# Kernel optimization log

Measured on AMD Instinct MI355X. Metric: run time of the kernel, lower is better.

## Reference

```python
import jax, jax.numpy as jnp
import numpy as np

KSIZE = 3; STRIDE = 1; RATE = 2; FUSE_K = 3; SCALE = 10.0; EPS = 1e-4
B, C, RH, RW = 2, 128, 80, 80  # raw (full-res) feature shape


def setup_inputs() -> dict:
    key = jax.random.key(0)
    ks = jax.random.split(key, 5)
    shp = (B, C, RH, RW)
    names = ["left", "right", "mid", "raw_left", "raw_right"]
    return {n: jax.random.normal(k, shp, dtype=jnp.float32) for n, k in zip(names, ks)}


def _same_pads(H, W, k, s):
    oh, ow = -(-H // s), -(-W // s)
    ph = max(0, (oh - 1) * s + k - H)
    pw = max(0, (ow - 1) * s + k - W)
    return ((ph // 2, ph - ph // 2), (pw // 2, pw - pw // 2))


def extract_patches(x, k, s):
    # torch extract_image_patches with 'same' padding -> (b, L, c, k, k)
    b, c, H, W = x.shape
    pads = _same_pads(H, W, k, s)
    p = jax.lax.conv_general_dilated_patches(x, (k, k), (s, s), pads)  # (b, c*k*k, oh, ow)
    oh, ow = p.shape[2], p.shape[3]
    p = p.reshape(b, c, k, k, oh * ow)  # feature dim is channel-major (c, k, k), like torch unfold
    return p.transpose(0, 4, 1, 2, 3)


def _fuse(s, Hl, Wl, Hm, Wm):
    # diagonal fuse-conv: conv of (b,1,L,P) score image with eye(k), twice with transposes
    b = s.shape[0]
    k = FUSE_K
    eye = jnp.eye(k, dtype=s.dtype).reshape(1, 1, k, k)
    pad = ((k // 2, k // 2), (k // 2, k // 2))
    conv = lambda x: jax.lax.conv_general_dilated(x, eye, (1, 1), pad)
    x = conv(s.reshape(b, 1, Hl * Wl, Hm * Wm))
    x = x.reshape(b, Hl, Wl, Hm, Wm).transpose(0, 2, 1, 4, 3).reshape(b, 1, Wl * Hl, Wm * Hm)
    x = conv(x)
    x = x.reshape(b, Wl, Hl, Wm, Hm).transpose(0, 2, 1, 4, 3)  # (b, Hl, Wl, Hm, Wm)
    return x.reshape(b, Hl * Wl, Hm, Wm)


def _deconv_one(attn, patches):
    # torch conv_transpose2d(attn, patches, stride=RATE, padding=1):
    # conv with lhs dilation RATE, spatially-flipped kernel, padding k-1-1
    kk = patches.shape[-1]
    rhs = jnp.flip(patches, (-2, -1)).transpose(1, 0, 2, 3)  # (C, L, kk, kk)
    p = kk - 1 - 1
    out = jax.lax.conv_general_dilated(attn[None], rhs, (1, 1), ((p, p), (p, p)),
                                       lhs_dilation=(RATE, RATE),
                                       dimension_numbers=('NCHW', 'OIHW', 'NCHW'))
    return out[0]


def _forward(left, right, mid, raw_left, raw_right):
    kernel = 2 * RATE
    rawp_l = extract_patches(raw_left, kernel, RATE * STRIDE)   # (B, L, C, 4, 4)
    rawp_r = extract_patches(raw_right, kernel, RATE * STRIDE)
    # nearest downsample by rate
    l = left[:, :, ::RATE, ::RATE]
    r = right[:, :, ::RATE, ::RATE]
    m = mid[:, :, ::RATE, ::RATE]
    Hl, Wl = l.shape[2], l.shape[3]
    Hm, Wm = m.shape[2], m.shape[3]
    lp = extract_patches(l, KSIZE, STRIDE)   # (B, L, C, 3, 3)
    rp = extract_patches(r, KSIZE, STRIDE)
    mp = extract_patches(m, KSIZE, STRIDE)   # (B, P, C, 3, 3); conv2d(same-padded xi, w) == patch dot

    def norm(p):
        # torch: sqrt(reduce_sum(p^2 + eps)) -- eps added elementwise before the sum
        return p / jnp.sqrt(jnp.sum(p * p + EPS, axis=(2, 3, 4), keepdims=True))

    sl = jnp.einsum('bqcij,bpcij->bqp', norm(lp), mp).reshape(-1, Hl * Wl, Hm, Wm)
    sr = jnp.einsum('bqcij,bpcij->bqp', norm(rp), mp).reshape(-1, Hl * Wl, Hm, Wm)
    sl = _fuse(sl, Hl, Wl, Hm, Wm)
    sr = _fuse(sr, Hl, Wl, Hm, Wm)
    al = jax.nn.softmax(sl * SCALE, axis=1)
    ar = jax.nn.softmax(sr * SCALE, axis=1)
    y_l = jax.vmap(_deconv_one)(al, rawp_l) / 4.0   # (B, C, RH, RW)
    y_r = jax.vmap(_deconv_one)(ar, rawp_r) / 4.0
    # cos_function_weight: cosine blending ramp along width (1 at left edge -> 0 at right edge)
    w = 0.5 * (1.0 + jnp.cos(jnp.pi * jnp.arange(RW, dtype=y_l.dtype) / (RW - 1)))
    w = w.reshape(1, 1, 1, RW)
    return w * y_l + jnp.flip(w, 3) * y_r


def reference(left, right, mid, raw_left, raw_right):
    return _forward(left, right, mid, raw_left, raw_right)
```

## Files before the change

kernel.cpp:

```cpp
#include <hip/hip_runtime.h>
#include <hip/hip_bf16.h>

typedef __hip_bfloat16 bf16;
typedef __attribute__((ext_vector_type(8))) short short8;
typedef __attribute__((ext_vector_type(4))) float f32x4;
typedef float f32x4u __attribute__((ext_vector_type(4), aligned(4)));
typedef unsigned short ushort_t;

#define PI_F 3.14159265358979323846f
#define GPAD_Z 3111696L

#define GLOAD_LDS16(gp, lp)                                                    \
  __builtin_amdgcn_global_load_lds(                                            \
      (const __attribute__((address_space(1))) unsigned int*)(gp),             \
      (__attribute__((address_space(3))) unsigned int*)(lp), 16, 0, 0)

__global__ __launch_bounds__(128) void prep_pt(const float* __restrict__ left,
                                               const float* __restrict__ right,
                                               const float* __restrict__ mid,
                                               bf16* __restrict__ PTe,
                                               bf16* __restrict__ MTe,
                                               float* __restrict__ SQ) {
  int q = blockIdx.x;
  int y = blockIdx.y;
  int c = threadIdx.x;
  int qi = q / 40, qj = q - qi * 40;
  const float* src;
  bf16* dst;
  int b;
  bool aside = (y < 4);
  if (aside) {
    b = y & 1;
    src = (y < 2) ? left : right;
    dst = PTe + (long)y * 1664 * 384;
  } else {
    b = y - 4;
    src = mid;
    dst = MTe + (long)(y - 4) * 1664 * 384;
  }
  float v = src[(((long)b * 128 + c) * 80 + 2 * qi) * 80 + 2 * qj];
  bf16 hi = __float2bfloat16(v);
  bf16 lo = __float2bfloat16(v - __bfloat162float(hi));
  if (aside) {
    dst[(long)q * 384 + c] = hi;
    dst[(long)q * 384 + 128 + c] = lo;
    dst[(long)q * 384 + 256 + c] = hi;
  } else {
    dst[(long)q * 384 + c] = hi;
    dst[(long)q * 384 + 128 + c] = hi;
    dst[(long)q * 384 + 256 + c] = lo;
  }
  if (aside) {
    __shared__ float red[128];
    red[c] = v * v;
    __syncthreads();
    for (int s = 64; s > 0; s >>= 1) {
      if (c < s) red[c] += red[c + s];
      __syncthreads();
    }
    if (c == 0) SQ[y * 1600 + q] = red[0];
  }
}

__global__ __launch_bounds__(256) void pad_invn_kernel(float* __restrict__ Gp,
                                                       const float* __restrict__ SQ,
                                                       float* __restrict__ INV) {
  int z = blockIdx.y;
  int bx = blockIdx.x;
  if (bx < 1764) {
    float* R = Gp + (long)z * GPAD_Z + (long)bx * 1764;
    int r42 = bx % 42;
    if (r42 == 0 || r42 == 41) {
      for (int c = threadIdx.x; c < 1764; c += 256) R[c] = 0.f;
    } else {
      for (int i = threadIdx.x; i < 84; i += 256) {
        int c = (i >> 1) * 42 + ((i & 1) ? 41 : 0);
        R[c] = 0.f;
      }
    }
  } else {
    int q = (bx - 1764) * 256 + threadIdx.x;
    if (q < 1600) {
      int qi = q / 40, qj = q - qi * 40;
      float s = 0.1152f;
      #pragma unroll
      for (int di = -1; di <= 1; ++di)
        #pragma unroll
        for (int dj = -1; dj <= 1; ++dj) {
          int a = qi + di, b2 = qj + dj;
          if (a >= 0 && a < 40 && b2 >= 0 && b2 < 40) s += SQ[z * 1600 + a * 40 + b2];
        }
      INV[z * 1600 + q] = rsqrtf(s);
    }
  }
}

__global__ __launch_bounds__(256) void gemm_nt(const bf16* __restrict__ A,
                                               const bf16* __restrict__ B,
                                               float* __restrict__ C,
                                               int M, int N, int K,
                                               long Az, long Bz, long Cz,
                                               int bmod, int cpad) {
  int z = blockIdx.z;
  A += (long)z * Az;
  B += (long)(bmod ? (z & 1) : z) * Bz;
  C += (long)z * Cz;
  __shared__ bf16 As[128 * 32];
  __shared__ bf16 Bs[128 * 32];
  int lane = threadIdx.x & 63;
  int w = threadIdx.x >> 6;
  int mb = blockIdx.x * 128;
  int nb = blockIdx.y * 128;
  int lr = lane >> 2;
  int gb = (lane & 3) ^ ((lane >> 3) & 3);
  int lm = lane & 15;
  int swz = (lm >> 1) & 3;
  int kb = lane >> 4;
  int pos = (kb ^ swz) * 8;
  int warow = (w >> 1) * 64;
  int wbrow = (w & 1) * 64;
  f32x4 acc[4][4];
  #pragma unroll
  for (int i = 0; i < 4; ++i)
    #pragma unroll
    for (int j = 0; j < 4; ++j) {
      f32x4 zv = {0.f, 0.f, 0.f, 0.f};
      acc[i][j] = zv;
    }
  for (int k0 = 0; k0 < K; k0 += 32) {
    __syncthreads();
    #pragma unroll
    for (int t = 0; t < 2; ++t) {
      int r = (w * 2 + t) * 16 + lr;
      GLOAD_LDS16(A + (long)(mb + r) * K + k0 + gb * 8, As + (w * 2 + t) * 512);
      GLOAD_LDS16(B + (long)(nb + r) * K + k0 + gb * 8, Bs + (w * 2 + t) * 512);
    }
    __syncthreads();
    short8 af[4], bfr[4];
    #pragma unroll
    for (int i = 0; i < 4; ++i) {
      af[i]  = *reinterpret_cast<const short8*>(As + (warow + i * 16 + lm) * 32 + pos);
      bfr[i] = *reinterpret_cast<const short8*>(Bs + (wbrow + i * 16 + lm) * 32 + pos);
    }
    #pragma unroll
    for (int i = 0; i < 4; ++i)
      #pragma unroll
      for (int j = 0; j < 4; ++j)
        acc[i][j] = __builtin_amdgcn_mfma_f32_16x16x32_bf16(af[i], bfr[j], acc[i][j], 0, 0, 0);
  }
  int m0 = mb + warow;
  int n0 = nb + wbrow;
  int col = lane & 15;
  int r0 = (lane >> 4) * 4;
  #pragma unroll
  for (int i = 0; i < 4; ++i)
    #pragma unroll
    for (int j = 0; j < 4; ++j) {
      int n = n0 + j * 16 + col;
      if (n < N) {
        int nc = cpad ? ((n / 40) * 42 + (n - (n / 40) * 40) + 43) : n;
        #pragma unroll
        for (int r = 0; r < 4; ++r) {
          int m = m0 + i * 16 + r0 + r;
          if (m < M) {
            long mr = cpad ? ((long)((m / 40) * 42 + (m - (m / 40) * 40) + 43) * 1764)
                           : ((long)m * N);
            C[mr + nc] = acc[i][j][r];
          }
        }
      }
    }
}

#define BAR() __builtin_amdgcn_s_barrier()
#define LGKM0() asm volatile("s_waitcnt lgkmcnt(0)" ::: "memory")
#define STAGE_A(tt, h)                                                         \
  { long _k = (long)(tt) * 64;                                                 \
    char* _d = lds + (((tt) & 1) << 16) + (((h) * 8 + w) << 11);               \
    GLOAD_LDS16(a_row[h] + _k, _d);                                            \
    GLOAD_LDS16(a_row[h] + _k + 32, _d + 1024); }
#define STAGE_B(tt, h)                                                         \
  { long _k = (long)(tt) * 64;                                                 \
    char* _d = lds + (((tt) & 1) << 16) + 32768 + (((h) * 8 + w) << 11);       \
    GLOAD_LDS16(b_row[h] + _k, _d);                                            \
    GLOAD_LDS16(b_row[h] + _k + 32, _d + 1024); }
#define LD8(off) (*reinterpret_cast<const short8*>(lds + (off)))
#define LOAD_A(dst, bufo, mh)                                                  \
  { _Pragma("unroll") for (int i = 0; i < 4; ++i)                              \
      { _Pragma("unroll") for (int kc = 0; kc < 2; ++kc)                       \
          dst[i][kc] = LD8((bufo) + (((wm * 8 + (mh) * 4 + i) * 2 + kc) << 10) + rd_off); } }
#define LOAD_B(dst, bufo, nh)                                                  \
  { _Pragma("unroll") for (int j = 0; j < 2; ++j)                              \
      { _Pragma("unroll") for (int kc = 0; kc < 2; ++kc)                       \
          dst[j][kc] = LD8((bufo) + 32768 + (((wn * 4 + (nh) * 2 + j) * 2 + kc) << 10) + rd_off); } }
#define MFMA16(arr, mh, nh, bset)                                              \
  { _Pragma("unroll") for (int kc = 0; kc < 2; ++kc)                           \
      { _Pragma("unroll") for (int i = 0; i < 4; ++i)                          \
          { _Pragma("unroll") for (int j = 0; j < 2; ++j)                      \
              acc[(mh) * 4 + i][(nh) * 2 + j] = __builtin_amdgcn_mfma_f32_16x16x32_bf16( \
                  arr[i][kc], bset[j][kc], acc[(mh) * 4 + i][(nh) * 2 + j], 0, 0, 0); } } }

__global__ __launch_bounds__(512, 2) void gemm256_nt(const bf16* __restrict__ A,
                                                     const bf16* __restrict__ B,
                                                     float* __restrict__ C,
                                                     int M, int N, int K,
                                                     long Az, long Bz, long Cz,
                                                     int nballoc) {
  __shared__ __align__(16) char lds[131072];
  int l = blockIdx.x + (blockIdx.y << 3) + blockIdx.z * 56;
  int x = l & 7;
  int j7 = l >> 3;
  int z = x >> 1;
  int mb = (((x & 1) << 2) + (j7 & 3)) * 256;
  int nb = (j7 >> 2) * 256;
  A += (long)z * Az;
  B += (long)z * Bz;
  C += (long)z * Cz;
  int tid = threadIdx.x;
  int lane = tid & 63;
  int w = tid >> 6;
  int wm = w >> 2;
  int wn = w & 3;
  int NT = K >> 6;

  int srcb = (lane << 4) ^ (lane & 32);
  int r_src = srcb >> 6;
  int c_src = (srcb & 63) >> 1;
  const bf16* a_row[2];
  const bf16* b_row[2];
  #pragma unroll
  for (int h = 0; h < 2; ++h) {
    a_row[h] = A + (long)(mb + (h * 8 + w) * 16 + r_src) * K + c_src;
    int br = nb + (h * 8 + w) * 16 + r_src;
    if (br > nballoc - 1) br = nballoc - 1;
    b_row[h] = B + (long)br * K + c_src;
  }
  int rd_off = (((lane & 15) << 6) | ((lane >> 4) << 4)) ^ ((lane & 8) << 2);

  short8 a[4][2], a2[4][2], p0[2][2], p1[2][2];
  f32x4 acc[8][4];
  #pragma unroll
  for (int i = 0; i < 8; ++i)
    #pragma unroll
    for (int j = 0; j < 4; ++j) {
      f32x4 zv = {0.f, 0.f, 0.f, 0.f};
      acc[i][j] = zv;
    }

  STAGE_A(0, 0); STAGE_A(0, 1); STAGE_B(0, 0); STAGE_B(0, 1);
  STAGE_A(1, 0); STAGE_A(1, 1); STAGE_B(1, 0);
  asm volatile("s_waitcnt vmcnt(6)" ::: "memory");
  BAR();

  for (int t = 0; t < NT; ++t) {
    int bufo = (t & 1) << 16;
    LOAD_A(a, bufo, 0);
    LOAD_B(p0, bufo, 0);
    LOAD_B(p1, bufo, 1);
    if (t + 1 < NT) STAGE_B(t + 1, 1);
    BAR(); LGKM0();
    __builtin_amdgcn_s_setprio(1); MFMA16(a, 0, 0, p0); __builtin_amdgcn_s_setprio(0);
    BAR();
    LOAD_A(a2, bufo, 1);
    BAR();
    __builtin_amdgcn_s_setprio(1); MFMA16(a, 0, 1, p1); __builtin_amdgcn_s_setprio(0);
    BAR();
    LGKM0();
    __builtin_amdgcn_s_setprio(1); MFMA16(a2, 1, 1, p1); __builtin_amdgcn_s_setprio(0);
    BAR();
    __builtin_amdgcn_s_setprio(1); MFMA16(a2, 1, 0, p0); __builtin_amdgcn_s_setprio(0);
    BAR();
    if (t + 2 < NT) {
      STAGE_A(t + 2, 0); STAGE_A(t + 2, 1); STAGE_B(t + 2, 0);
      asm volatile("s_waitcnt vmcnt(6)" ::: "memory");
      BAR();
    } else if (t + 1 < NT) {
      asm volatile("s_waitcnt vmcnt(0)" ::: "memory");
      BAR();
    }
  }

  int col = lane & 15;
  int r0 = (lane >> 4) * 4;
  int m_base = mb + wm * 128;
  int n_base = nb + wn * 64;
  #pragma unroll
  for (int i = 0; i < 8; ++i)
    #pragma unroll
    for (int j = 0; j < 4; ++j) {
      int n = n_base + j * 16 + col;
      if (n < N) {
        #pragma unroll
        for (int r = 0; r < 4; ++r) {
          int m = m_base + i * 16 + r0 + r;
          C[(long)m * N + n] = acc[i][j][r];
        }
      }
    }
}

__device__ __forceinline__ float ps9(const float* __restrict__ Gz, int q2, int p2) {
  int qi2 = q2 / 40, qj2 = q2 - qi2 * 40;
  int pi2 = p2 / 40, pj2 = p2 - pi2 * 40;
  const float* base = Gz + (long)(qi2 * 42 + qj2 + 43) * 1764 + (pi2 * 42 + pj2 + 43);
  float t = 0.f;
  #pragma unroll
  for (int di = -1; di <= 1; ++di)
    #pragma unroll
    for (int dj = -1; dj <= 1; ++dj)
      t += base[(long)(di * 42 + dj) * 1765];
  return t;
}

__global__ __launch_bounds__(256) void s1fuse1_fast(const float* __restrict__ Gp,
                                                    const float* __restrict__ INV,
                                                    float* __restrict__ S2) {
  __shared__ float Hs[23][176];
  __shared__ float IVs[21];
  int b = blockIdx.x;
  int g = b % 10;
  int half = (b / 10) & 1;
  int qi = (b / 20) % 40;
  int z = b / 800;
  int qj0 = half ? 20 : 1;
  int tau0 = qj0 - 2;
  int colL = 168 * g + 39;
  const float* Gz = Gp + (long)z * GPAD_Z;
  const float* IVz = INV + z * 1600;
  int tid = threadIdx.x;

  for (int idx = tid; idx < 23 * 44; idx += 256) {
    int row = idx / 44;
    int cv = idx - row * 44;
    int gr = qi * 42 + 43 + tau0 + row;
    int gc = colL + 4 * cv;
    const float* p1 = Gz + (long)gr * 1764 + gc;
    f32x4 v = *(const f32x4u*)(p1 - 42 * 1765) + *(const f32x4u*)(p1)
            + *(const f32x4u*)(p1 + 42 * 1765);
    *reinterpret_cast<f32x4*>(&Hs[row][4 * cv]) = v;
  }
  if (tid < 21) IVs[tid] = IVz[qi * 40 + qj0 - 1 + tid];
  __syncthreads();

  for (int j = tid; j < 760; j += 256) {
    int jq = j / 40;
    int jp = j - jq * 40;
    int pblk = jp / 10;
    int pj0 = (jp - pblk * 10) * 4;
    int C0loc = pblk * 42 + pj0 + 4;
    int p0 = g * 160 + jp * 4;
    int qj = qj0 + jq;
    int q = qi * 40 + qj;
    f32x4 hs[5];
    #pragma unroll
    for (int s2 = 0; s2 < 5; ++s2) {
      int tr = jq + s2;
      int cc = C0loc + s2 - 2;
      f32x4 hv = {Hs[tr][cc], Hs[tr][cc + 1], Hs[tr][cc + 2], Hs[tr][cc + 3]};
      hs[s2] = hv;
    }
    f32x4 c12 = hs[1] + hs[2];
    f32x4 c23 = hs[2] + hs[3];
    f32x4 psm = hs[0] + c12;
    f32x4 ps0 = c12 + hs[3];
    f32x4 psp = c23 + hs[4];
    if (pj0 == 0) {
      float pv = 0.f;
      if (p0 >= 1) {
        int C2 = pblk * 42 + 1;
        #pragma unroll
        for (int dj = -1; dj <= 1; ++dj) pv += Hs[jq + 1 + dj][C2 + dj];
      }
      psm[0] = pv;
    } else if (pj0 == 36) {
      float pv = 0.f;
      if (p0 + 4 < 1600) {
        int C2 = pblk * 42 + 46;
        #pragma unroll
        for (int dj = -1; dj <= 1; ++dj) pv += Hs[jq + 3 + dj][C2 + dj];
      }
      psp[3] = pv;
    }
    float wm = IVs[jq], w0 = IVs[jq + 1], wp = IVs[jq + 2];
    f32x4 outv = psm * wm + ps0 * w0 + psp * wp;
    *reinterpret_cast<f32x4*>(S2 + ((long)z * 1600 + q) * 1600 + p0) = outv;
  }
}

__global__ __launch_bounds__(256) void s1fuse1_slow(const float* __restrict__ Gp,
                                                    const float* __restrict__ INV,
                                                    float* __restrict__ S2) {
  int z = blockIdx.y;
  unsigned int gid = blockIdx.x * 256u + threadIdx.x;
  int qidx = gid / 400u;
  int quad = gid - qidx * 400u;
  int qi = qidx >> 1;
  int qj = (qidx & 1) * 39;
  int q = qi * 40 + qj;
  int p0 = quad * 4;
  const float* Gz = Gp + (long)z * GPAD_Z;
  const float* IVz = INV + z * 1600;
  f32x4 outv;
  #pragma unroll
  for (int t = 0; t < 4; ++t) {
    int p = p0 + t;
    float s = 0.f;
    #pragma unroll
    for (int d = -1; d <= 1; ++d) {
      int q2 = q + d, p2 = p + d;
      bool ok = ((unsigned)q2 < 1600u) && ((unsigned)p2 < 1600u);
      if (ok) s += IVz[q2] * ps9(Gz, q2, p2);
    }
    outv[t] = s;
  }
  *reinterpret_cast<f32x4*>(S2 + ((long)z * 1600 + q) * 1600 + p0) = outv;
}

__global__ __launch_bounds__(256) void fuse2_kernel(const float* __restrict__ S2,
                                                    float* __restrict__ S3) {
  int z = blockIdx.y;
  int bx = blockIdx.x;
  int xc = bx & 7, rest = bx >> 3;
  int lid = (xc < 4 ? xc * 313 : 1252 + (xc - 4) * 312) + rest;
  unsigned int gid = (unsigned int)lid * 256u + threadIdx.x;
  int q = gid / 400u;
  int quad = gid - q * 400u;
  int p0 = quad * 4;
  const float* S = S2 + (long)z * 2560000;
  int il = q / 40, jl = q - il * 40;
  int im = p0 / 40, jm = p0 - im * 40;
  int u = jl * 40 + il;
  f32x4 acc = {0.f, 0.f, 0.f, 0.f};
  #pragma unroll
  for (int d = -1; d <= 1; ++d) {
    int u2 = u + d;
    if ((unsigned)u2 >= 1600u) continue;
    int q2 = (u2 % 40) * 40 + u2 / 40;
    int imd = im + d;
    if ((unsigned)imd < 40u) {
      acc += *reinterpret_cast<const f32x4*>(S + (long)q2 * 1600 + imd * 40 + jm);
    } else {
      #pragma unroll
      for (int t = 0; t < 4; ++t) {
        int v2 = (jm + t) * 40 + im + d;
        if ((unsigned)v2 < 1600u) {
          int p2 = (v2 % 40) * 40 + v2 / 40;
          acc[t] += S[(long)q2 * 1600 + p2];
        }
      }
    }
  }
  *reinterpret_cast<f32x4*>(S3 + ((long)z * 1600 + q) * 1600 + p0) = acc;
}

__global__ __launch_bounds__(256) void smax_part(const float* __restrict__ S3,
                                                 float* __restrict__ Pm,
                                                 float* __restrict__ Ps) {
  int z = blockIdx.z, qc = blockIdx.y;
  int pl = threadIdx.x & 63;
  int ql = threadIdx.x >> 6;
  int p = blockIdx.x * 64 + pl;
  const float* S = S3 + (long)z * 2560000;
  float m = -1e30f, s = 0.f;
  for (int i = 0; i < 50; ++i) {
    int q = qc * 200 + i * 4 + ql;
    float x = 10.f * S[(long)q * 1600 + p];
    if (x > m) { s *= __expf(m - x); m = x; }
    s += __expf(x - m);
  }
  __shared__ float lm[4][64], ls[4][64];
  lm[ql][pl] = m;
  ls[ql][pl] = s;
  __syncthreads();
  if (ql == 0) {
    float M = m, SS = s;
    #pragma unroll
    for (int j = 1; j < 4; ++j) {
      float mj = lm[j][pl], sj = ls[j][pl];
      if (mj > M) { SS = SS * __expf(M - mj) + sj; M = mj; }
      else SS += sj * __expf(mj - M);
    }
    Pm[((long)z * 8 + qc) * 1600 + p] = M;
    Ps[((long)z * 8 + qc) * 1600 + p] = SS;
  }
}

__global__ __launch_bounds__(256) void smax_write(const float* __restrict__ S3,
                                                  const float* __restrict__ Pm,
                                                  const float* __restrict__ Ps,
                                                  bf16* __restrict__ AT) {
  int z = blockIdx.z;
  int p0 = blockIdx.x * 64, q0 = blockIdx.y * 64;
  int pl = threadIdx.x & 63, ql = threadIdx.x >> 6;
  __shared__ float lfm[64], lfs[64];
  if (ql == 0) {
    int p = p0 + pl;
    float M = -1e30f;
    #pragma unroll
    for (int c = 0; c < 8; ++c) M = fmaxf(M, Pm[((long)z * 8 + c) * 1600 + p]);
    float S = 0.f;
    #pragma unroll
    for (int c = 0; c < 8; ++c)
      S += Ps[((long)z * 8 + c) * 1600 + p] * __expf(Pm[((long)z * 8 + c) * 1600 + p] - M);
    lfm[pl] = M;
    lfs[pl] = 1.f / S;
  }
  __syncthreads();
  __shared__ ushort_t T[64][66];
  float fm = lfm[pl];
  float fs = lfs[pl];
  const float* S = S3 + (long)z * 2560000;
  #pragma unroll
  for (int i = 0; i < 16; ++i) {
    int qq = ql + i * 4;
    float x = 10.f * S[(long)(q0 + qq) * 1600 + p0 + pl];
    bf16 h = __float2bfloat16(__expf(x - fm) * fs);
    T[pl][qq] = *reinterpret_cast<ushort_t*>(&h);
  }
  __syncthreads();
  int rp = threadIdx.x >> 5;
  int j = threadIdx.x & 31;
  #pragma unroll
  for (int pass = 0; pass < 8; ++pass) {
    int row = pass * 8 + rp;
    unsigned int vv = (unsigned int)T[row][2 * j] | ((unsigned int)T[row][2 * j + 1] << 16);
    *reinterpret_cast<unsigned int*>(AT + ((long)z * 1664 + p0 + row) * 1600 + q0 + 2 * j) = vv;
  }
}

__global__ __launch_bounds__(256) void rawpt_kernel(const float* __restrict__ rawL,
                                                    const float* __restrict__ rawR,
                                                    bf16* __restrict__ RAWPT) {
  int z = blockIdx.z;
  int r = blockIdx.y * 4 + (threadIdx.x >> 6);
  int q = blockIdx.x * 64 + (threadIdx.x & 63);
  const float* raw = ((z < 2) ? rawL : rawR) + (long)(z & 1) * 819200;
  int c = r >> 4, i = (r >> 2) & 3, j = r & 3;
  int qi = q / 40, qj = q - qi * 40;
  int y = 2 * qi + i - 1, x = 2 * qj + j - 1;
  float v = 0.f;
  if (y >= 0 && y < 80 && x >= 0 && x < 80) v = raw[((long)c * 80 + y) * 80 + x];
  RAWPT[((long)z * 2048 + r) * 1600 + q] = __float2bfloat16(v);
}

__global__ __launch_bounds__(256) void paste_kernel(const float* __restrict__ Z,
                                                    float* __restrict__ out) {
  int t8 = blockIdx.x * 256 + threadIdx.x;
  int g = t8 % 10;
  int r = t8 / 10;
  int x0 = g * 8;
  int h = x0 >> 1;
  int y = r % 80;
  int cc = (r / 80) % 128;
  int b = r / (80 * 128);
  int imA = (y - 1) >> 1, ipA = y - 2 * imA + 1;
  const long zs = 2048L * 1600;
  const float* ZL = Z + (long)b * zs;
  const float* ZR = Z + (long)(2 + b) * zs;
  f32x4 EL = {0.f,0.f,0.f,0.f}, OL = {0.f,0.f,0.f,0.f};
  f32x4 ER = {0.f,0.f,0.f,0.f}, OR_ = {0.f,0.f,0.f,0.f};
  #pragma unroll
  for (int a = 0; a < 2; ++a) {
    int im = imA + a;
    if ((unsigned)im > 39u) continue;
    int ip = ipA - 2 * a;
    long rb = (long)(cc * 16 + ip * 4) * 1600 + im * 40;
    f32x4 l3 = *(const f32x4u*)(ZL + rb + 3 * 1600 + h - 1);
    f32x4 l1 = *(const f32x4u*)(ZL + rb + 1 * 1600 + h);
    f32x4 l2 = *(const f32x4u*)(ZL + rb + 2 * 1600 + h);
    f32x4 l0 = *(const f32x4u*)(ZL + rb + 0 * 1600 + h + 1);
    f32x4 r3 = *(const f32x4u*)(ZR + rb + 3 * 1600 + h - 1);
    f32x4 r1 = *(const f32x4u*)(ZR + rb + 1 * 1600 + h);
    f32x4 r2 = *(const f32x4u*)(ZR + rb + 2 * 1600 + h);
    f32x4 r0 = *(const f32x4u*)(ZR + rb + 0 * 1600 + h + 1);
    if (x0 == 0) { l3[0] = 0.f; r3[0] = 0.f; }
    if (x0 == 72) { l0[3] = 0.f; r0[3] = 0.f; }
    EL += l3 + l1; OL += l2 + l0;
    ER += r3 + r1; OR_ += r2 + r0;
  }
  f32x4 o0, o1;
  #pragma unroll
  for (int k = 0; k < 4; ++k) {
    int xe = x0 + 2 * k, xo = xe + 1;
    float ce = cosf(PI_F * xe / 79.f);
    float co = cosf(PI_F * xo / 79.f);
    float ve = 0.25f * (0.5f * (1.f + ce) * EL[k] + 0.5f * (1.f - ce) * ER[k]);
    float vo = 0.25f * (0.5f * (1.f + co) * OL[k] + 0.5f * (1.f - co) * OR_[k]);
    if (k < 2) { o0[2 * k] = ve; o0[2 * k + 1] = vo; }
    else { o1[2 * (k - 2)] = ve; o1[2 * (k - 2) + 1] = vo; }
  }
  float* dst = out + (long)r * 80 + x0;
  *reinterpret_cast<f32x4*>(dst) = o0;
  *reinterpret_cast<f32x4*>(dst + 4) = o1;
}

extern "C" void kernel_launch(void* const* d_in, const int* in_sizes, int n_in,
                              void* d_out, int out_size, void* d_ws, size_t ws_size,
                              hipStream_t stream) {
  const float* left  = (const float*)d_in[0];
  const float* right = (const float*)d_in[1];
  const float* mid   = (const float*)d_in[2];
  const float* rawL  = (const float*)d_in[3];
  const float* rawR  = (const float*)d_in[4];
  float* out = (float*)d_out;
  char* ws = (char*)d_ws;

  bf16*  PTe   = (bf16*)(ws + 0);
  bf16*  MTe   = (bf16*)(ws + 5111808);
  float* SQ    = (float*)(ws + 7667712);
  float* INV   = (float*)(ws + 7693312);
  float* Pm    = (float*)(ws + 7718912);
  float* Ps    = (float*)(ws + 7923712);
  float* X     = (float*)(ws + 8179712);
  float* Y     = (float*)(ws + 60608512);
  bf16*  AT    = (bf16*)(ws + 101568512);
  bf16*  RAWPT = (bf16*)Y;

  prep_pt<<<dim3(1600, 6, 1), 128, 0, stream>>>(left, right, mid, PTe, MTe, SQ);
  pad_invn_kernel<<<dim3(1771, 4), 256, 0, stream>>>(X, SQ, INV);
  gemm_nt<<<dim3(13, 13, 4), 256, 0, stream>>>(PTe, MTe, X, 1600, 1600, 384,
                                               1664L * 384, 1664L * 384, GPAD_Z, 1, 1);
  s1fuse1_fast<<<3200, 256, 0, stream>>>(X, INV, Y);
  s1fuse1_slow<<<dim3(125, 4), 256, 0, stream>>>(X, INV, Y);
  fuse2_kernel<<<dim3(2500, 4), 256, 0, stream>>>(Y, X);
  smax_part<<<dim3(25, 8, 4), 256, 0, stream>>>(X, Pm, Ps);
  smax_write<<<dim3(25, 25, 4), 256, 0, stream>>>(X, Pm, Ps, AT);
  rawpt_kernel<<<dim3(25, 512, 4), 256, 0, stream>>>(rawL, rawR, RAWPT);
  gemm256_nt<<<dim3(8, 7, 4), 512, 0, stream>>>(RAWPT, AT, X, 2048, 1600, 1600,
                                                2048L * 1600, 1664L * 1600, 2048L * 1600, 1664);
  paste_kernel<<<800, 256, 0, stream>>>(X, out);
}
```

Measured before the change: 299.9 us.

## Interleave global-to-LDS staging with MFMA phases and remap LDS tile layout

Changes the LDS row layout for the A and B tiles so that each half-tile (mh/nh) occupies a contiguous region, and staging warps write rows matching that layout. The main loop now spreads the next-tile global_load_lds issues across the four MFMA phases instead of batching them at the end, and reuses one A register set instead of two. The aim is to overlap global memory traffic with compute and reduce register pressure. In exchange, the vmcnt accounting and the barrier placement become more delicate, and any mismatch risks read-after-write hazards on the LDS buffers.

After: 296.9 us. Within noise of the previous version (-1.0%).

```diff
diff --git a/kernel.cpp b/kernel.cpp
--- a/kernel.cpp
+++ b/kernel.cpp
@@ -188,11 +188,11 @@
 #define LOAD_A(dst, bufo, mh)                                                  \
   { _Pragma("unroll") for (int i = 0; i < 4; ++i)                              \
       { _Pragma("unroll") for (int kc = 0; kc < 2; ++kc)                       \
-          dst[i][kc] = LD8((bufo) + (((wm * 8 + (mh) * 4 + i) * 2 + kc) << 10) + rd_off); } }
+          dst[i][kc] = LD8((bufo) + ((((mh) * 8 + wm * 4 + i) * 2 + kc) << 10) + rd_off); } }
 #define LOAD_B(dst, bufo, nh)                                                  \
   { _Pragma("unroll") for (int j = 0; j < 2; ++j)                              \
       { _Pragma("unroll") for (int kc = 0; kc < 2; ++kc)                       \
-          dst[j][kc] = LD8((bufo) + 32768 + (((wn * 4 + (nh) * 2 + j) * 2 + kc) << 10) + rd_off); } }
+          dst[j][kc] = LD8((bufo) + 32768 + ((((nh) * 8 + wn * 2 + j) * 2 + kc) << 10) + rd_off); } }
 #define MFMA16(arr, mh, nh, bset)                                              \
   { _Pragma("unroll") for (int kc = 0; kc < 2; ++kc)                           \
       { _Pragma("unroll") for (int i = 0; i < 4; ++i)                          \
@@ -230,14 +230,16 @@
   const bf16* b_row[2];
   #pragma unroll
   for (int h = 0; h < 2; ++h) {
-    a_row[h] = A + (long)(mb + (h * 8 + w) * 16 + r_src) * K + c_src;
-    int br = nb + (h * 8 + w) * 16 + r_src;
+    int ga = (w >> 2) * 8 + (w & 3) + h * 4;
+    a_row[h] = A + (long)(mb + ga * 16 + r_src) * K + c_src;
+    int gB = (w >> 1) * 4 + (w & 1) + h * 2;
+    int br = nb + gB * 16 + r_src;
     if (br > nballoc - 1) br = nballoc - 1;
     b_row[h] = B + (long)br * K + c_src;
   }
   int rd_off = (((lane & 15) << 6) | ((lane >> 4) << 4)) ^ ((lane & 8) << 2);
 
-  short8 a[4][2], a2[4][2], p0[2][2], p1[2][2];
+  short8 a[4][2], p0[2][2], p1[2][2];
   f32x4 acc[8][4];
   #pragma unroll
   for (int i = 0; i < 8; ++i)
@@ -248,7 +250,7 @@
     }
 
   STAGE_A(0, 0); STAGE_A(0, 1); STAGE_B(0, 0); STAGE_B(0, 1);
-  STAGE_A(1, 0); STAGE_A(1, 1); STAGE_B(1, 0);
+  STAGE_A(1, 0); STAGE_B(1, 0); STAGE_A(1, 1);
   asm volatile("s_waitcnt vmcnt(6)" ::: "memory");
   BAR();
 
@@ -256,28 +258,28 @@
     int bufo = (t & 1) << 16;
     LOAD_A(a, bufo, 0);
     LOAD_B(p0, bufo, 0);
-    LOAD_B(p1, bufo, 1);
     if (t + 1 < NT) STAGE_B(t + 1, 1);
     BAR(); LGKM0();
     __builtin_amdgcn_s_setprio(1); MFMA16(a, 0, 0, p0); __builtin_amdgcn_s_setprio(0);
     BAR();
-    LOAD_A(a2, bufo, 1);
-    BAR();
+    LOAD_B(p1, bufo, 1);
+    if (t + 2 < NT) STAGE_A(t + 2, 0);
+    BAR(); LGKM0();
     __builtin_amdgcn_s_setprio(1); MFMA16(a, 0, 1, p1); __builtin_amdgcn_s_setprio(0);
     BAR();
-    LGKM0();
-    __builtin_amdgcn_s_setprio(1); MFMA16(a2, 1, 1, p1); __builtin_amdgcn_s_setprio(0);
-    BAR();
-    __builtin_amdgcn_s_setprio(1); MFMA16(a2, 1, 0, p0); __builtin_amdgcn_s_setprio(0);
+    LOAD_A(a, bufo, 1);
+    if (t + 2 < NT) STAGE_B(t + 2, 0);
+    BAR(); LGKM0();
+    __builtin_amdgcn_s_setprio(1); MFMA16(a, 1, 0, p0); __builtin_amdgcn_s_setprio(0);
     BAR();
     if (t + 2 < NT) {
-      STAGE_A(t + 2, 0); STAGE_A(t + 2, 1); STAGE_B(t + 2, 0);
+      STAGE_A(t + 2, 1);
       asm volatile("s_waitcnt vmcnt(6)" ::: "memory");
-      BAR();
     } else if (t + 1 < NT) {
       asm volatile("s_waitcnt vmcnt(0)" ::: "memory");
-      BAR();
-    }
+    }
+    __builtin_amdgcn_s_setprio(1); MFMA16(a, 1, 1, p1); __builtin_amdgcn_s_setprio(0);
+    BAR();
   }
 
   int col = lane & 15;
```
